# Kernel tuning notes

Hardware: AMD Instinct MI355X
Metric: run time of the kernel (lower is better)

## Reference

```python
import jax, jax.numpy as jnp
import numpy as np

N_NODES = 100000
N_EDGES = 1600000
IN_C, HID_C, OUT_C = 128, 128, 64


def setup_inputs() -> dict:
    key = jax.random.key(0)
    ks = jax.random.split(key, 9)
    features = jax.random.normal(ks[0], (N_NODES, IN_C), dtype=jnp.float32)
    src = jax.random.randint(ks[1], (N_EDGES,), 0, N_NODES, dtype=jnp.int32)
    dst = jax.random.randint(ks[2], (N_EDGES,), 0, N_NODES, dtype=jnp.int32)
    def glorot(k, fan_in, fan_out):
        lim = float(np.sqrt(6.0 / (fan_in + fan_out)))
        return jax.random.uniform(k, (fan_in, fan_out), jnp.float32, -lim, lim)
    return {
        "features": features, "src": src, "dst": dst,
        "W1": glorot(ks[3], IN_C, HID_C), "b1": jnp.zeros((HID_C,), jnp.float32),
        "W2": glorot(ks[4], HID_C, HID_C), "b2": jnp.zeros((HID_C,), jnp.float32),
        "W3": glorot(ks[5], HID_C, OUT_C), "b3": jnp.zeros((OUT_C,), jnp.float32),
    }


def _graph_conv(x, src, dst, W, b, inv_sqrt_out, inv_sqrt_in):
    # DGL GraphConv, norm='both': h = D_in^{-1/2} A D_out^{-1/2} (x W) + b
    h = (x * inv_sqrt_out[:, None]) @ W            # [N, out]
    agg = jax.ops.segment_sum(h[src], dst, num_segments=N_NODES)
    return agg * inv_sqrt_in[:, None] + b


def reference(features, src, dst, W1, b1, W2, b2, W3, b3):
    ones = jnp.ones((N_EDGES,), jnp.float32)
    deg_out = jnp.clip(jax.ops.segment_sum(ones, src, num_segments=N_NODES), 1.0)
    deg_in = jnp.clip(jax.ops.segment_sum(ones, dst, num_segments=N_NODES), 1.0)
    iso, isi = deg_out ** -0.5, deg_in ** -0.5
    x = jax.nn.relu(_graph_conv(features, src, dst, W1, b1, iso, isi))
    x = jax.nn.relu(_graph_conv(x, src, dst, W2, b2, iso, isi))
    x = _graph_conv(x, src, dst, W3, b3, iso, isi)
    return jax.nn.log_softmax(x, axis=1)
```

## Files before the change

### kernel.cpp

```cpp
#include <hip/hip_runtime.h>
#include <hip/hip_bf16.h>

#define IN_C 128
#define HID_C 128
#define OUT_C 64

typedef unsigned short u16;
typedef unsigned int   u32;
typedef __attribute__((ext_vector_type(8))) short short8;
typedef __attribute__((ext_vector_type(4))) float f32x4;

__device__ __forceinline__ u16 bf16_bits(float x) {
    __hip_bfloat16 h = __float2bfloat16(x);
    return *(u16*)&h;
}
__device__ __forceinline__ void split_hi_lo(float a, u16& hi, u16& lo) {
    __hip_bfloat16 h = __float2bfloat16(a);
    float hf = __bfloat162float(h);
    __hip_bfloat16 l = __float2bfloat16(a - hf);
    hi = *(u16*)&h; lo = *(u16*)&l;
}


__global__ __launch_bounds__(256)
void part_hist(const int* __restrict__ keys, int* __restrict__ bh,
               int E, int K, int NB) {
    const int b = blockIdx.x;
    extern __shared__ int lh[];
    for (int i = threadIdx.x; i < K; i += 256) lh[i] = 0;
    __syncthreads();
    const int lo = (int)((long long)E * b / NB);
    const int hi = (int)((long long)E * (b + 1) / NB);
    for (int i = lo + threadIdx.x; i < hi; i += 256)
        atomicAdd(&lh[keys[i] >> 8], 1);
    __syncthreads();
    for (int k = threadIdx.x; k < K; k += 256)
        bh[k * NB + b] = lh[k];
}

template <bool PACK>
__global__ __launch_bounds__(256)
void part_scatter(const int* __restrict__ keys, const int* __restrict__ other,
                  const int* __restrict__ ofs, u32* __restrict__ out,
                  int E, int K, int NB) {
    const int b = blockIdx.x;
    extern __shared__ int lcur[];
    for (int k = threadIdx.x; k < K; k += 256) lcur[k] = ofs[k * NB + b];
    __syncthreads();
    const int lo = (int)((long long)E * b / NB);
    const int hi = (int)((long long)E * (b + 1) / NB);
    for (int i = lo + threadIdx.x; i < hi; i += 256) {
        int key = keys[i];
        int p = atomicAdd(&lcur[key >> 8], 1);
        out[p] = PACK ? (((u32)other[i] << 8) | (u32)(key & 255)) : (u32)key;
    }
}

__global__ __launch_bounds__(256)
void bucket_count(const u32* __restrict__ pairs, const int* __restrict__ ofs,
                  int* __restrict__ cnt, int N, int NB, int K, int cap) {
    const int k = blockIdx.x;
    __shared__ int lc[256];
    lc[threadIdx.x] = 0;
    __syncthreads();
    const int s0 = ofs[k * NB];
    const int s1 = (k == K - 1) ? cap : ofs[(k + 1) * NB];
    for (int i = s0 + threadIdx.x; i < s1; i += 256)
        atomicAdd(&lc[pairs[i] & 255], 1);
    __syncthreads();
    const int node = k * 256 + threadIdx.x;
    if (node < N) cnt[node] = lc[threadIdx.x];
}

__global__ __launch_bounds__(256)
void bucket_fill(const u32* __restrict__ pairs, const int* __restrict__ ofs,
                 const int* __restrict__ row_start, int* __restrict__ csr,
                 int N, int NB, int K, int E) {
    const int k = blockIdx.x;
    __shared__ int lcur[256];
    const int node = k * 256 + threadIdx.x;
    lcur[threadIdx.x] = (node < N) ? row_start[node] : 0;
    __syncthreads();
    const int s0 = ofs[k * NB];
    const int s1 = (k == K - 1) ? E : ofs[(k + 1) * NB];
    for (int i = s0 + threadIdx.x; i < s1; i += 256) {
        u32 pr = pairs[i];
        int p = atomicAdd(&lcur[pr & 255], 1);
        csr[p] = (int)(pr >> 8);
    }
}


__global__ __launch_bounds__(256)
void scan_pass1(const int* __restrict__ in, int* __restrict__ blocksum, int M) {
    const int b = blockIdx.x, t = threadIdx.x;
    const int base = b * 1024 + t * 4;
    int s = 0;
#pragma unroll
    for (int j = 0; j < 4; ++j) {
        int idx = base + j;
        if (idx < M) s += in[idx];
    }
#pragma unroll
    for (int off = 32; off >= 1; off >>= 1) s += __shfl_xor(s, off);
    __shared__ int wsum[4];
    if ((t & 63) == 0) wsum[t >> 6] = s;
    __syncthreads();
    if (t == 0) blocksum[b] = wsum[0] + wsum[1] + wsum[2] + wsum[3];
}

__global__ __launch_bounds__(1024)
void scan_g2(int* __restrict__ a, int nb) {
    __shared__ int s[1024];
    const int t = threadIdx.x;
    int v = (t < nb) ? a[t] : 0;
    s[t] = v;
    __syncthreads();
    for (int off = 1; off < 1024; off <<= 1) {
        int x = (t >= off) ? s[t - off] : 0;
        __syncthreads();
        s[t] += x;
        __syncthreads();
    }
    if (t < nb) a[t] = s[t] - v;
}

__global__ __launch_bounds__(256)
void scan_g3(const int* __restrict__ in, const int* __restrict__ blockoff,
             int* __restrict__ out, int M) {
    __shared__ int ssum[256];
    const int b = blockIdx.x, t = threadIdx.x;
    const int base = b * 1024 + t * 4;
    int c[4];
#pragma unroll
    for (int j = 0; j < 4; ++j) {
        int idx = base + j;
        c[j] = (idx < M) ? in[idx] : 0;
    }
    const int tot = c[0] + c[1] + c[2] + c[3];
    ssum[t] = tot;
    __syncthreads();
    for (int off = 1; off < 256; off <<= 1) {
        int v = (t >= off) ? ssum[t - off] : 0;
        __syncthreads();
        ssum[t] += v;
        __syncthreads();
    }
    int run = blockoff[b] + ssum[t] - tot;
#pragma unroll
    for (int j = 0; j < 4; ++j) {
        int idx = base + j;
        if (idx < M) { out[idx] = run; run += c[j]; }
    }
}

__global__ __launch_bounds__(256)
void scan_pass3n(const int* __restrict__ cnt_in, const int* __restrict__ cnt_out,
                 const int* __restrict__ blockoff, int* __restrict__ row_start,
                 float* __restrict__ iso, float* __restrict__ isi, int N, int E) {
    __shared__ int ssum[256];
    const int b = blockIdx.x, t = threadIdx.x;
    const int base = b * 1024 + t * 4;
    int c[4];
#pragma unroll
    for (int j = 0; j < 4; ++j) {
        int idx = base + j;
        c[j] = (idx < N) ? cnt_in[idx] : 0;
    }
    const int tot = c[0] + c[1] + c[2] + c[3];
    ssum[t] = tot;
    __syncthreads();
    for (int off = 1; off < 256; off <<= 1) {
        int v = (t >= off) ? ssum[t - off] : 0;
        __syncthreads();
        ssum[t] += v;
        __syncthreads();
    }
    int run = blockoff[b] + ssum[t] - tot;
#pragma unroll
    for (int j = 0; j < 4; ++j) {
        int idx = base + j;
        if (idx < N) {
            row_start[idx] = run;
            run += c[j];
            int di = c[j] < 1 ? 1 : c[j];
            int co = cnt_out[idx];
            int dd = co < 1 ? 1 : co;
            isi[idx] = rsqrtf((float)di);
            iso[idx] = rsqrtf((float)dd);
        }
    }
    if (b == 0 && t == 0) row_start[N] = E;
}


__global__ __launch_bounds__(128)
void wt_prep(const float* __restrict__ W, u16* __restrict__ Wt, int C) {
    const int c = blockIdx.x, k = threadIdx.x;
    Wt[c * 128 + k] = bf16_bits(W[k * C + c]);
}

__global__ __launch_bounds__(256)
void x_prep(const float* __restrict__ X, const float* __restrict__ iso,
            u16* __restrict__ Ah, u16* __restrict__ Al, int total ) {
    for (int i = blockIdx.x * 256 + threadIdx.x; i < total; i += gridDim.x * 256) {
        int row = i >> 5;
        float s = iso[row];
        float4 x = ((const float4*)X)[i];
        u16 h0, l0, h1, l1, h2, l2, h3, l3;
        split_hi_lo(x.x * s, h0, l0);
        split_hi_lo(x.y * s, h1, l1);
        split_hi_lo(x.z * s, h2, l2);
        split_hi_lo(x.w * s, h3, l3);
        uint2 hp = make_uint2((u32)h0 | ((u32)h1 << 16), (u32)h2 | ((u32)h3 << 16));
        uint2 lp = make_uint2((u32)l0 | ((u32)l1 << 16), (u32)l2 | ((u32)l3 << 16));
        ((uint2*)Ah)[i] = hp;
        ((uint2*)Al)[i] = lp;
    }
}

template <int C>
__global__ __launch_bounds__(256)
void gemm_mfma(const u16* __restrict__ Ah, const u16* __restrict__ Al,
               const u16* __restrict__ Wt, u16* __restrict__ H, int N) {
    constexpr int NT = C / 16;
    __shared__ u16 sAh[64 * 136];
    __shared__ u16 sAl[64 * 136];
    const int t = threadIdx.x;
    const int row0 = blockIdx.x * 64;

    for (int c = t; c < 1024; c += 256) {
        int r = c >> 4, kc = c & 15;
        int gr = row0 + r;
        if (gr >= N) gr = N - 1;
        *(uint4*)(&sAh[r * 136 + kc * 8]) = *(const uint4*)(Ah + (size_t)gr * 128 + kc * 8);
        *(uint4*)(&sAl[r * 136 + kc * 8]) = *(const uint4*)(Al + (size_t)gr * 128 + kc * 8);
    }
    __syncthreads();

    const int wid = t >> 6, lane = t & 63;
    const int r0 = wid * 16;
    const int arow = r0 + (lane & 15);
    const int kb = (lane >> 4) * 8;

    f32x4 acc[NT];
#pragma unroll
    for (int i = 0; i < NT; ++i) acc[i] = (f32x4){0.f, 0.f, 0.f, 0.f};

    const u16* wbase = Wt + (size_t)(lane & 15) * 128 + kb;

#pragma unroll
    for (int kk = 0; kk < 4; ++kk) {
        short8 ah = *(const short8*)(&sAh[arow * 136 + kk * 32 + kb]);
        short8 al = *(const short8*)(&sAl[arow * 136 + kk * 32 + kb]);
#pragma unroll
        for (int ct = 0; ct < NT; ++ct) {
            short8 bf = *(const short8*)(wbase + ct * 16 * 128 + kk * 32);
            acc[ct] = __builtin_amdgcn_mfma_f32_16x16x32_bf16(ah, bf, acc[ct], 0, 0, 0);
            acc[ct] = __builtin_amdgcn_mfma_f32_16x16x32_bf16(al, bf, acc[ct], 0, 0, 0);
        }
    }

    const int rbase = row0 + r0 + (lane >> 4) * 4;
#pragma unroll
    for (int ct = 0; ct < NT; ++ct) {
        int gcol = ct * 16 + (lane & 15);
#pragma unroll
        for (int r = 0; r < 4; ++r) {
            int grow = rbase + r;
            if (grow < N) H[(size_t)grow * C + gcol] = bf16_bits(acc[ct][r]);
        }
    }
}


__global__ __launch_bounds__(256)
void agg_relu(const u16* __restrict__ H, const int* __restrict__ row_start,
              const int* __restrict__ csr_src, const float* __restrict__ isi,
              const float* __restrict__ iso, const float* __restrict__ bias,
              u16* __restrict__ Ah, u16* __restrict__ Al, int N) {
    const int wid  = (int)((blockIdx.x * (size_t)blockDim.x + threadIdx.x) >> 6);
    const int lane = threadIdx.x & 63;
    if (wid >= N) return;
    const int rs = row_start[wid];
    const int re = row_start[wid + 1];
    const float sc = isi[wid];

    float ax = 0.f, ay = 0.f;
    int e = rs;
    while (e < re) {
        int nloc = re - e;
        if (nloc > 64) nloc = 64;
        int idx = 0;
        if (lane < nloc) idx = csr_src[e + lane];
        int j = 0;
        for (; j + 4 <= nloc; j += 4) {
            int s0 = __builtin_amdgcn_readlane(idx, j);
            int s1 = __builtin_amdgcn_readlane(idx, j + 1);
            int s2 = __builtin_amdgcn_readlane(idx, j + 2);
            int s3 = __builtin_amdgcn_readlane(idx, j + 3);
            u32 v0 = *(const u32*)(H + (size_t)s0 * 128 + lane * 2);
            u32 v1 = *(const u32*)(H + (size_t)s1 * 128 + lane * 2);
            u32 v2 = *(const u32*)(H + (size_t)s2 * 128 + lane * 2);
            u32 v3 = *(const u32*)(H + (size_t)s3 * 128 + lane * 2);
            ax += __uint_as_float(v0 << 16); ay += __uint_as_float(v0 & 0xffff0000u);
            ax += __uint_as_float(v1 << 16); ay += __uint_as_float(v1 & 0xffff0000u);
            ax += __uint_as_float(v2 << 16); ay += __uint_as_float(v2 & 0xffff0000u);
            ax += __uint_as_float(v3 << 16); ay += __uint_as_float(v3 & 0xffff0000u);
        }
        for (; j < nloc; ++j) {
            int s0 = __builtin_amdgcn_readlane(idx, j);
            u32 v0 = *(const u32*)(H + (size_t)s0 * 128 + lane * 2);
            ax += __uint_as_float(v0 << 16); ay += __uint_as_float(v0 & 0xffff0000u);
        }
        e += nloc;
    }
    float2 b = *(const float2*)(bias + lane * 2);
    float o0 = fmaxf(ax * sc + b.x, 0.f);
    float o1 = fmaxf(ay * sc + b.y, 0.f);
    const float so = iso[wid];
    u16 h0, l0, h1, l1;
    split_hi_lo(o0 * so, h0, l0);
    split_hi_lo(o1 * so, h1, l1);
    ((u32*)Ah)[(size_t)wid * 64 + lane] = (u32)h0 | ((u32)h1 << 16);
    ((u32*)Al)[(size_t)wid * 64 + lane] = (u32)l0 | ((u32)l1 << 16);
}

__global__ __launch_bounds__(256)
void agg_final(const u16* __restrict__ H, const int* __restrict__ row_start,
               const int* __restrict__ csr_src, const float* __restrict__ isi,
               const float* __restrict__ bias, float* __restrict__ Out, int N) {
    const int wid  = (int)((blockIdx.x * (size_t)blockDim.x + threadIdx.x) >> 6);
    const int lane = threadIdx.x & 63;
    if (wid >= N) return;
    const int rs = row_start[wid];
    const int re = row_start[wid + 1];
    const float sc = isi[wid];

    float a = 0.f;
    int e = rs;
    while (e < re) {
        int nloc = re - e;
        if (nloc > 64) nloc = 64;
        int idx = 0;
        if (lane < nloc) idx = csr_src[e + lane];
        int j = 0;
        for (; j + 4 <= nloc; j += 4) {
            int s0 = __builtin_amdgcn_readlane(idx, j);
            int s1 = __builtin_amdgcn_readlane(idx, j + 1);
            int s2 = __builtin_amdgcn_readlane(idx, j + 2);
            int s3 = __builtin_amdgcn_readlane(idx, j + 3);
            u32 v0 = H[(size_t)s0 * 64 + lane];
            u32 v1 = H[(size_t)s1 * 64 + lane];
            u32 v2 = H[(size_t)s2 * 64 + lane];
            u32 v3 = H[(size_t)s3 * 64 + lane];
            a += __uint_as_float(v0 << 16);
            a += __uint_as_float(v1 << 16);
            a += __uint_as_float(v2 << 16);
            a += __uint_as_float(v3 << 16);
        }
        for (; j < nloc; ++j) {
            int s0 = __builtin_amdgcn_readlane(idx, j);
            a += __uint_as_float((u32)H[(size_t)s0 * 64 + lane] << 16);
        }
        e += nloc;
    }
    float v = a * sc + bias[lane];
    float m = v;
#pragma unroll
    for (int off = 32; off >= 1; off >>= 1) m = fmaxf(m, __shfl_xor(m, off));
    float ex = expf(v - m);
    float ss = ex;
#pragma unroll
    for (int off = 32; off >= 1; off >>= 1) ss += __shfl_xor(ss, off);
    v = (v - m) - logf(ss);
    Out[(size_t)wid * 64 + lane] = v;
}


extern "C" void kernel_launch(void* const* d_in, const int* in_sizes, int n_in,
                              void* d_out, int out_size, void* d_ws, size_t ws_size,
                              hipStream_t stream) {
    const float* features = (const float*)d_in[0];
    const int*   src      = (const int*)d_in[1];
    const int*   dst      = (const int*)d_in[2];
    const float* W1       = (const float*)d_in[3];
    const float* b1       = (const float*)d_in[4];
    const float* W2       = (const float*)d_in[5];
    const float* b2       = (const float*)d_in[6];
    const float* W3       = (const float*)d_in[7];
    const float* b3       = (const float*)d_in[8];
    float*       out      = (float*)d_out;

    const int N  = in_sizes[0] / IN_C;
    const int E  = in_sizes[1];
    const int K  = (N + 255) >> 8;
    const int NB = 256;
    const int M  = 2 * K * NB;
    const int nbe = (M + 1023) / 1024;
    const int nb  = (N + 1023) / 1024;

    char* ws = (char*)d_ws;
    const size_t SLOT = 400128;
    int*   cnt_out   = (int*)(ws + 0 * SLOT);
    int*   cnt_in    = (int*)(ws + 1 * SLOT);
    int*   row_start = (int*)(ws + 2 * SLOT);
    float* iso       = (float*)(ws + 3 * SLOT);
    float* isi       = (float*)(ws + 4 * SLOT);
    int*   blocksum  = (int*)(ws + 5 * SLOT);
    int*   eblocksum = blocksum + 2048;
    int*   csr       = (int*)(ws + 6 * SLOT);
    char*  p         = ws + 6 * SLOT + 6400000;
    int*   BH        = (int*)p;
    int*   OFS       = (int*)(p + 1000000);
    u32*   pairs     = (u32*)(p + 2000000);
    u16*   Hb        = (u16*)(p + 14800000);
    u16*   Ah        = (u16*)(p + 40400000);
    u16*   Al        = (u16*)(p + 66000000);
    u16*   Wt1       = (u16*)(p + 91600000);
    u16*   Wt2       = Wt1 + 128 * 128;
    u16*   Wt3       = Wt2 + 128 * 128;

    const size_t ldsK = (size_t)K * sizeof(int);

    part_hist<<<NB, 256, ldsK, stream>>>(dst, BH,           E, K, NB);
    part_hist<<<NB, 256, ldsK, stream>>>(src, BH + K * NB,  E, K, NB);
    scan_pass1<<<nbe, 256, 0, stream>>>(BH, eblocksum, M);
    scan_g2<<<1, 1024, 0, stream>>>(eblocksum, nbe);
    scan_g3<<<nbe, 256, 0, stream>>>(BH, eblocksum, OFS, M);
    part_scatter<true ><<<NB, 256, ldsK, stream>>>(dst, src, OFS,          pairs, E, K, NB);
    part_scatter<false><<<NB, 256, ldsK, stream>>>(src, src, OFS + K * NB, pairs, E, K, NB);
    bucket_count<<<K, 256, 0, stream>>>(pairs, OFS,          cnt_in,  N, NB, K, E);
    bucket_count<<<K, 256, 0, stream>>>(pairs, OFS + K * NB, cnt_out, N, NB, K, 2 * E);
    scan_pass1<<<nb, 256, 0, stream>>>(cnt_in, blocksum, N);
    scan_g2<<<1, 1024, 0, stream>>>(blocksum, nb);
    scan_pass3n<<<nb, 256, 0, stream>>>(cnt_in, cnt_out, blocksum, row_start, iso, isi, N, E);
    bucket_fill<<<K, 256, 0, stream>>>(pairs, OFS, row_start, csr, N, NB, K, E);

    wt_prep<<<128, 128, 0, stream>>>(W1, Wt1, 128);
    wt_prep<<<128, 128, 0, stream>>>(W2, Wt2, 128);
    wt_prep<<<64,  128, 0, stream>>>(W3, Wt3, 64);
    x_prep<<<2048, 256, 0, stream>>>(features, iso, Ah, Al, N * 32);

    const int gblocks = (N + 63) / 64;
    const int ablocks = (int)(((size_t)N * 64 + 255) / 256);

    gemm_mfma<128><<<gblocks, 256, 0, stream>>>(Ah, Al, Wt1, Hb, N);
    agg_relu<<<ablocks, 256, 0, stream>>>(Hb, row_start, csr, isi, iso, b1, Ah, Al, N);
    gemm_mfma<128><<<gblocks, 256, 0, stream>>>(Ah, Al, Wt2, Hb, N);
    agg_relu<<<ablocks, 256, 0, stream>>>(Hb, row_start, csr, isi, iso, b2, Ah, Al, N);
    gemm_mfma<64><<<gblocks, 256, 0, stream>>>(Ah, Al, Wt3, Hb, N);
    agg_final<<<ablocks, 256, 0, stream>>>(Hb, row_start, csr, isi, b3, out, N);
}
```

Measured before the change: 397.7 us.

## Fuse aggregation with next-layer GEMM and fold input prep into first GEMM

Aggregation for layers 1 and 2 now writes its ReLU'd, scaled hi/lo bf16 rows straight into shared memory, and the same block then runs the MFMA GEMM for the next layer. This removes the Ah/Al global round trips and several launches. Input splitting is folded into the first GEMM, and the three weight-prep launches become one. Gathers are unrolled to 8 and use packed f32 adds. The trade-off is that each wave now handles 16 rows serially in the aggregation, giving fewer in-flight waves per node and a block barrier before the GEMM.

```diff
diff --git a/kernel.cpp b/kernel.cpp
--- a/kernel.cpp
+++ b/kernel.cpp
@@ -9,6 +9,7 @@
 typedef unsigned int   u32;
 typedef __attribute__((ext_vector_type(8))) short short8;
 typedef __attribute__((ext_vector_type(4))) float f32x4;
+typedef __attribute__((ext_vector_type(2))) float f32x2;
 
 __device__ __forceinline__ u16 bf16_bits(float x) {
     __hip_bfloat16 h = __float2bfloat16(x);
@@ -19,6 +20,12 @@
     float hf = __bfloat162float(h);
     __hip_bfloat16 l = __float2bfloat16(a - hf);
     hi = *(u16*)&h; lo = *(u16*)&l;
+}
+__device__ __forceinline__ void pk_acc(f32x2& acc, u32 v) {
+    f32x2 val;
+    val.x = __uint_as_float(v << 16);
+    val.y = __uint_as_float(v & 0xffff0000u);
+    asm("v_pk_add_f32 %0, %0, %1" : "+v"(acc) : "v"(val));
 }
 
 
@@ -195,18 +202,110 @@
 
 
 __global__ __launch_bounds__(128)
-void wt_prep(const float* __restrict__ W, u16* __restrict__ Wt, int C) {
-    const int c = blockIdx.x, k = threadIdx.x;
-    Wt[c * 128 + k] = bf16_bits(W[k * C + c]);
-}
-
-__global__ __launch_bounds__(256)
-void x_prep(const float* __restrict__ X, const float* __restrict__ iso,
-            u16* __restrict__ Ah, u16* __restrict__ Al, int total ) {
-    for (int i = blockIdx.x * 256 + threadIdx.x; i < total; i += gridDim.x * 256) {
-        int row = i >> 5;
-        float s = iso[row];
-        float4 x = ((const float4*)X)[i];
+void wt_prep_all(const float* __restrict__ W1, const float* __restrict__ W2,
+                 const float* __restrict__ W3, u16* __restrict__ Wt1,
+                 u16* __restrict__ Wt2, u16* __restrict__ Wt3) {
+    const int b = blockIdx.x, k = threadIdx.x;
+    if (b < 128)       Wt1[b * 128 + k] = bf16_bits(W1[k * 128 + b]);
+    else if (b < 256)  { int c = b - 128; Wt2[c * 128 + k] = bf16_bits(W2[k * 128 + c]); }
+    else               { int c = b - 256; Wt3[c * 128 + k] = bf16_bits(W3[k * 64 + c]); }
+}
+
+template <int C>
+__device__ __forceinline__
+void mfma_store(const u16* sAh, const u16* sAl, const u16* __restrict__ Wt,
+                u16* __restrict__ H, int row0, int N, int t) {
+    constexpr int NT = C / 16;
+    const int wid = t >> 6, lane = t & 63;
+    const int r0 = wid * 16;
+    const int arow = r0 + (lane & 15);
+    const int kb = (lane >> 4) * 8;
+
+    f32x4 acc[NT];
+#pragma unroll
+    for (int i = 0; i < NT; ++i) acc[i] = (f32x4){0.f, 0.f, 0.f, 0.f};
+
+    const u16* wbase = Wt + (size_t)(lane & 15) * 128 + kb;
+
+#pragma unroll
+    for (int kk = 0; kk < 4; ++kk) {
+        short8 ah = *(const short8*)(&sAh[arow * 136 + kk * 32 + kb]);
+        short8 al = *(const short8*)(&sAl[arow * 136 + kk * 32 + kb]);
+#pragma unroll
+        for (int ct = 0; ct < NT; ++ct) {
+            short8 bf = *(const short8*)(wbase + ct * 16 * 128 + kk * 32);
+            acc[ct] = __builtin_amdgcn_mfma_f32_16x16x32_bf16(ah, bf, acc[ct], 0, 0, 0);
+            acc[ct] = __builtin_amdgcn_mfma_f32_16x16x32_bf16(al, bf, acc[ct], 0, 0, 0);
+        }
+    }
+
+    const int rbase = row0 + r0 + (lane >> 4) * 4;
+#pragma unroll
+    for (int ct = 0; ct < NT; ++ct) {
+        int gcol = ct * 16 + (lane & 15);
+#pragma unroll
+        for (int r = 0; r < 4; ++r) {
+            int grow = rbase + r;
+            if (grow < N) H[(size_t)grow * C + gcol] = bf16_bits(acc[ct][r]);
+        }
+    }
+}
+
+
+__device__ __forceinline__
+f32x2 gather128(const u16* __restrict__ Hin, const int* __restrict__ csr_src,
+                int rs, int re, int lane) {
+    f32x2 acc; acc.x = 0.f; acc.y = 0.f;
+    int e = rs;
+    while (e < re) {
+        int nloc = re - e;
+        if (nloc > 64) nloc = 64;
+        int idx = (lane < nloc) ? csr_src[e + lane] : 0;
+        int j = 0;
+        for (; j + 8 <= nloc; j += 8) {
+            u32 v[8];
+#pragma unroll
+            for (int q = 0; q < 8; ++q) {
+                int s = __builtin_amdgcn_readlane(idx, j + q);
+                v[q] = *(const u32*)(Hin + (size_t)s * 128 + lane * 2);
+            }
+#pragma unroll
+            for (int q = 0; q < 8; ++q) pk_acc(acc, v[q]);
+        }
+        for (; j + 4 <= nloc; j += 4) {
+            u32 v[4];
+#pragma unroll
+            for (int q = 0; q < 4; ++q) {
+                int s = __builtin_amdgcn_readlane(idx, j + q);
+                v[q] = *(const u32*)(Hin + (size_t)s * 128 + lane * 2);
+            }
+#pragma unroll
+            for (int q = 0; q < 4; ++q) pk_acc(acc, v[q]);
+        }
+        for (; j < nloc; ++j) {
+            int s = __builtin_amdgcn_readlane(idx, j);
+            pk_acc(acc, *(const u32*)(Hin + (size_t)s * 128 + lane * 2));
+        }
+        e += nloc;
+    }
+    return acc;
+}
+
+
+__global__ __launch_bounds__(256)
+void gemm1_fused(const float* __restrict__ X, const float* __restrict__ iso,
+                 const u16* __restrict__ Wt, u16* __restrict__ H, int N) {
+    __shared__ u16 sAh[64 * 136];
+    __shared__ u16 sAl[64 * 136];
+    const int t = threadIdx.x;
+    const int row0 = blockIdx.x * 64;
+
+    for (int i = t; i < 2048; i += 256) {
+        int r = i >> 5, kv = (i & 31) << 2;
+        int gr = row0 + r;
+        if (gr >= N) gr = N - 1;
+        float s = iso[gr];
+        float4 x = *(const float4*)(X + (size_t)gr * 128 + kv);
         u16 h0, l0, h1, l1, h2, l2, h3, l3;
         split_hi_lo(x.x * s, h0, l0);
         split_hi_lo(x.y * s, h1, l1);
@@ -214,117 +313,46 @@
         split_hi_lo(x.w * s, h3, l3);
         uint2 hp = make_uint2((u32)h0 | ((u32)h1 << 16), (u32)h2 | ((u32)h3 << 16));
         uint2 lp = make_uint2((u32)l0 | ((u32)l1 << 16), (u32)l2 | ((u32)l3 << 16));
-        ((uint2*)Ah)[i] = hp;
-        ((uint2*)Al)[i] = lp;
-    }
-}
+        *(uint2*)(&sAh[r * 136 + kv]) = hp;
+        *(uint2*)(&sAl[r * 136 + kv]) = lp;
+    }
+    __syncthreads();
+    mfma_store<128>(sAh, sAl, Wt, H, row0, N, t);
+}
+
 
 template <int C>
 __global__ __launch_bounds__(256)
-void gemm_mfma(const u16* __restrict__ Ah, const u16* __restrict__ Al,
-               const u16* __restrict__ Wt, u16* __restrict__ H, int N) {
-    constexpr int NT = C / 16;
+void agg_gemm(const u16* __restrict__ Hin, const int* __restrict__ row_start,
+              const int* __restrict__ csr_src, const float* __restrict__ isi,
+              const float* __restrict__ iso, const float* __restrict__ bias,
+              const u16* __restrict__ Wt, u16* __restrict__ Hout, int N) {
     __shared__ u16 sAh[64 * 136];
     __shared__ u16 sAl[64 * 136];
-    const int t = threadIdx.x;
+    const int t = threadIdx.x, wid = t >> 6, lane = t & 63;
     const int row0 = blockIdx.x * 64;
-
-    for (int c = t; c < 1024; c += 256) {
-        int r = c >> 4, kc = c & 15;
-        int gr = row0 + r;
-        if (gr >= N) gr = N - 1;
-        *(uint4*)(&sAh[r * 136 + kc * 8]) = *(const uint4*)(Ah + (size_t)gr * 128 + kc * 8);
-        *(uint4*)(&sAl[r * 136 + kc * 8]) = *(const uint4*)(Al + (size_t)gr * 128 + kc * 8);
-    }
-    __syncthreads();
-
-    const int wid = t >> 6, lane = t & 63;
-    const int r0 = wid * 16;
-    const int arow = r0 + (lane & 15);
-    const int kb = (lane >> 4) * 8;
-
-    f32x4 acc[NT];
-#pragma unroll
-    for (int i = 0; i < NT; ++i) acc[i] = (f32x4){0.f, 0.f, 0.f, 0.f};
-
-    const u16* wbase = Wt + (size_t)(lane & 15) * 128 + kb;
-
-#pragma unroll
-    for (int kk = 0; kk < 4; ++kk) {
-        short8 ah = *(const short8*)(&sAh[arow * 136 + kk * 32 + kb]);
-        short8 al = *(const short8*)(&sAl[arow * 136 + kk * 32 + kb]);
-#pragma unroll
-        for (int ct = 0; ct < NT; ++ct) {
-            short8 bf = *(const short8*)(wbase + ct * 16 * 128 + kk * 32);
-            acc[ct] = __builtin_amdgcn_mfma_f32_16x16x32_bf16(ah, bf, acc[ct], 0, 0, 0);
-            acc[ct] = __builtin_amdgcn_mfma_f32_16x16x32_bf16(al, bf, acc[ct], 0, 0, 0);
-        }
-    }
-
-    const int rbase = row0 + r0 + (lane >> 4) * 4;
-#pragma unroll
-    for (int ct = 0; ct < NT; ++ct) {
-        int gcol = ct * 16 + (lane & 15);
-#pragma unroll
-        for (int r = 0; r < 4; ++r) {
-            int grow = rbase + r;
-            if (grow < N) H[(size_t)grow * C + gcol] = bf16_bits(acc[ct][r]);
-        }
-    }
-}
-
-
-__global__ __launch_bounds__(256)
-void agg_relu(const u16* __restrict__ H, const int* __restrict__ row_start,
-              const int* __restrict__ csr_src, const float* __restrict__ isi,
-              const float* __restrict__ iso, const float* __restrict__ bias,
-              u16* __restrict__ Ah, u16* __restrict__ Al, int N) {
-    const int wid  = (int)((blockIdx.x * (size_t)blockDim.x + threadIdx.x) >> 6);
-    const int lane = threadIdx.x & 63;
-    if (wid >= N) return;
-    const int rs = row_start[wid];
-    const int re = row_start[wid + 1];
-    const float sc = isi[wid];
-
-    float ax = 0.f, ay = 0.f;
-    int e = rs;
-    while (e < re) {
-        int nloc = re - e;
-        if (nloc > 64) nloc = 64;
-        int idx = 0;
-        if (lane < nloc) idx = csr_src[e + lane];
-        int j = 0;
-        for (; j + 4 <= nloc; j += 4) {
-            int s0 = __builtin_amdgcn_readlane(idx, j);
-            int s1 = __builtin_amdgcn_readlane(idx, j + 1);
-            int s2 = __builtin_amdgcn_readlane(idx, j + 2);
-            int s3 = __builtin_amdgcn_readlane(idx, j + 3);
-            u32 v0 = *(const u32*)(H + (size_t)s0 * 128 + lane * 2);
-            u32 v1 = *(const u32*)(H + (size_t)s1 * 128 + lane * 2);
-            u32 v2 = *(const u32*)(H + (size_t)s2 * 128 + lane * 2);
-            u32 v3 = *(const u32*)(H + (size_t)s3 * 128 + lane * 2);
-            ax += __uint_as_float(v0 << 16); ay += __uint_as_float(v0 & 0xffff0000u);
-            ax += __uint_as_float(v1 << 16); ay += __uint_as_float(v1 & 0xffff0000u);
-            ax += __uint_as_float(v2 << 16); ay += __uint_as_float(v2 & 0xffff0000u);
-            ax += __uint_as_float(v3 << 16); ay += __uint_as_float(v3 & 0xffff0000u);
-        }
-        for (; j < nloc; ++j) {
-            int s0 = __builtin_amdgcn_readlane(idx, j);
-            u32 v0 = *(const u32*)(H + (size_t)s0 * 128 + lane * 2);
-            ax += __uint_as_float(v0 << 16); ay += __uint_as_float(v0 & 0xffff0000u);
-        }
-        e += nloc;
-    }
-    float2 b = *(const float2*)(bias + lane * 2);
-    float o0 = fmaxf(ax * sc + b.x, 0.f);
-    float o1 = fmaxf(ay * sc + b.y, 0.f);
-    const float so = iso[wid];
-    u16 h0, l0, h1, l1;
-    split_hi_lo(o0 * so, h0, l0);
-    split_hi_lo(o1 * so, h1, l1);
-    ((u32*)Ah)[(size_t)wid * 64 + lane] = (u32)h0 | ((u32)h1 << 16);
-    ((u32*)Al)[(size_t)wid * 64 + lane] = (u32)l0 | ((u32)l1 << 16);
-}
+    const float2 b2 = *(const float2*)(bias + lane * 2);
+
+    for (int i = 0; i < 16; ++i) {
+        int r = wid * 16 + i;
+        int n = row0 + r;
+        if (n < N) {
+            int rs = row_start[n], re = row_start[n + 1];
+            f32x2 acc = gather128(Hin, csr_src, rs, re, lane);
+            float sc = isi[n], so = iso[n];
+            float o0 = fmaxf(acc.x * sc + b2.x, 0.f) * so;
+            float o1 = fmaxf(acc.y * sc + b2.y, 0.f) * so;
+            u16 h0, l0, h1, l1;
+            split_hi_lo(o0, h0, l0);
+            split_hi_lo(o1, h1, l1);
+            *(u32*)(&sAh[r * 136 + lane * 2]) = (u32)h0 | ((u32)h1 << 16);
+            *(u32*)(&sAl[r * 136 + lane * 2]) = (u32)l0 | ((u32)l1 << 16);
+        }
+    }
+    __syncthreads();
+    mfma_store<C>(sAh, sAl, Wt, Hout, row0, N, t);
+}
+
 
 __global__ __launch_bounds__(256)
 void agg_final(const u16* __restrict__ H, const int* __restrict__ row_start,
@@ -342,26 +370,31 @@
     while (e < re) {
         int nloc = re - e;
         if (nloc > 64) nloc = 64;
-        int idx = 0;
-        if (lane < nloc) idx = csr_src[e + lane];
+        int idx = (lane < nloc) ? csr_src[e + lane] : 0;
         int j = 0;
+        for (; j + 8 <= nloc; j += 8) {
+            u32 v[8];
+#pragma unroll
+            for (int q = 0; q < 8; ++q) {
+                int s = __builtin_amdgcn_readlane(idx, j + q);
+                v[q] = H[(size_t)s * 64 + lane];
+            }
+#pragma unroll
+            for (int q = 0; q < 8; ++q) a += __uint_as_float(v[q] << 16);
+        }
         for (; j + 4 <= nloc; j += 4) {
-            int s0 = __builtin_amdgcn_readlane(idx, j);
-            int s1 = __builtin_amdgcn_readlane(idx, j + 1);
-            int s2 = __builtin_amdgcn_readlane(idx, j + 2);
-            int s3 = __builtin_amdgcn_readlane(idx, j + 3);
-            u32 v0 = H[(size_t)s0 * 64 + lane];
-            u32 v1 = H[(size_t)s1 * 64 + lane];
-            u32 v2 = H[(size_t)s2 * 64 + lane];
-            u32 v3 = H[(size_t)s3 * 64 + lane];
-            a += __uint_as_float(v0 << 16);
-            a += __uint_as_float(v1 << 16);
-            a += __uint_as_float(v2 << 16);
-            a += __uint_as_float(v3 << 16);
+            u32 v[4];
+#pragma unroll
+            for (int q = 0; q < 4; ++q) {
+                int s = __builtin_amdgcn_readlane(idx, j + q);
+                v[q] = H[(size_t)s * 64 + lane];
+            }
+#pragma unroll
+            for (int q = 0; q < 4; ++q) a += __uint_as_float(v[q] << 16);
         }
         for (; j < nloc; ++j) {
-            int s0 = __builtin_amdgcn_readlane(idx, j);
-            a += __uint_as_float((u32)H[(size_t)s0 * 64 + lane] << 16);
+            int s = __builtin_amdgcn_readlane(idx, j);
+            a += __uint_as_float((u32)H[(size_t)s * 64 + lane] << 16);
         }
         e += nloc;
     }
@@ -414,10 +447,9 @@
     int*   BH        = (int*)p;
     int*   OFS       = (int*)(p + 1000000);
     u32*   pairs     = (u32*)(p + 2000000);
-    u16*   Hb        = (u16*)(p + 14800000);
-    u16*   Ah        = (u16*)(p + 40400000);
-    u16*   Al        = (u16*)(p + 66000000);
-    u16*   Wt1       = (u16*)(p + 91600000);
+    u16*   Hb1       = (u16*)(p + 14800000);
+    u16*   Hb2       = (u16*)(p + 40400000);
+    u16*   Wt1       = (u16*)(p + 66000000);
     u16*   Wt2       = Wt1 + 128 * 128;
     u16*   Wt3       = Wt2 + 128 * 128;
 
@@ -437,18 +469,13 @@
     scan_pass3n<<<nb, 256, 0, stream>>>(cnt_in, cnt_out, blocksum, row_start, iso, isi, N, E);
     bucket_fill<<<K, 256, 0, stream>>>(pairs, OFS, row_start, csr, N, NB, K, E);
 
-    wt_prep<<<128, 128, 0, stream>>>(W1, Wt1, 128);
-    wt_prep<<<128, 128, 0, stream>>>(W2, Wt2, 128);
-    wt_prep<<<64,  128, 0, stream>>>(W3, Wt3, 64);
-    x_prep<<<2048, 256, 0, stream>>>(features, iso, Ah, Al, N * 32);
+    wt_prep_all<<<320, 128, 0, stream>>>(W1, W2, W3, Wt1, Wt2, Wt3);
 
     const int gblocks = (N + 63) / 64;
     const int ablocks = (int)(((size_t)N * 64 + 255) / 256);
 
-    gemm_mfma<128><<<gblocks, 256, 0, stream>>>(Ah, Al, Wt1, Hb, N);
-    agg_relu<<<ablocks, 256, 0, stream>>>(Hb, row_start, csr, isi, iso, b1, Ah, Al, N);
-    gemm_mfma<128><<<gblocks, 256, 0, stream>>>(Ah, Al, Wt2, Hb, N);
-    agg_relu<<<ablocks, 256, 0, stream>>>(Hb, row_start, csr, isi, iso, b2, Ah, Al, N);
-    gemm_mfma<64><<<gblocks, 256, 0, stream>>>(Ah, Al, Wt3, Hb, N);
-    agg_final<<<ablocks, 256, 0, stream>>>(Hb, row_start, csr, isi, b3, out, N);
-}
+    gemm1_fused<<<gblocks, 256, 0, stream>>>(features, iso, Wt1, Hb1, N);
+    agg_gemm<128><<<gblocks, 256, 0, stream>>>(Hb1, row_start, csr, isi, iso, b1, Wt2, Hb2, N);
+    agg_gemm<64><<<gblocks, 256, 0, stream>>>(Hb2, row_start, csr, isi, iso, b2, Wt3, Hb1, N);
+    agg_final<<<ablocks, 256, 0, stream>>>(Hb1, row_start, csr, isi, b3, out, N);
+}
```

After: 427.2 us. +7.4%, slower.
